# Kernel optimization log

Measured on AMD Instinct MI355X. Metric: run time of the kernel, lower is better.

Reference implementation:

```python
import jax, jax.numpy as jnp
import numpy as np

N_NODES = 20000
N_EDGES = 320000
IN_DIM = 256
OUT_DIM = 256
H1, H2 = 640, 320


def _linear_params(key, fan_in, fan_out):
    k1, k2 = jax.random.split(key)
    bound = 1.0 / np.sqrt(fan_in)
    w = jax.random.uniform(k1, (fan_in, fan_out), minval=-bound, maxval=bound, dtype=jnp.float32)
    b = jax.random.uniform(k2, (fan_out,), minval=-bound, maxval=bound, dtype=jnp.float32)
    return w, b


def setup_inputs() -> dict:
    key = jax.random.key(0)
    ks = jax.random.split(key, 10)
    features = jax.random.normal(ks[0], (N_NODES, IN_DIM), dtype=jnp.float32)
    edge_index = jax.random.randint(ks[1], (2, N_EDGES), 0, N_NODES, dtype=jnp.int64)
    w1a, b1a = _linear_params(ks[2], IN_DIM, H1)
    w1b, b1b = _linear_params(ks[3], H1, H1)
    w2a, b2a = _linear_params(ks[4], H1, H2)
    w2b, b2b = _linear_params(ks[5], H2, H2)
    w3a, b3a = _linear_params(ks[6], H2, OUT_DIM)
    w3b, b3b = _linear_params(ks[7], OUT_DIM, OUT_DIM)
    wr, br = _linear_params(ks[8], IN_DIM, OUT_DIM)
    return dict(features=features, edge_index=edge_index,
                w1a=w1a, b1a=b1a, w1b=w1b, b1b=b1b,
                w2a=w2a, b2a=b2a, w2b=w2b, b2b=b2b,
                w3a=w3a, b3a=b3a, w3b=w3b, b3b=b3b,
                wr=wr, br=br)


def _gin_layer(x, src, dst, wa, ba, wb, bb):
    # DGL GINConv 'sum': h = (1+eps)*x + sum_{src->dst} x[src], eps=0
    agg = jax.ops.segment_sum(x[src], dst, num_segments=N_NODES)
    h = x + agg
    h = jax.nn.elu(h @ wa + ba)
    h = jax.nn.elu(h @ wb + bb)
    return h


def reference(features, edge_index, w1a, b1a, w1b, b1b, w2a, b2a, w2b, b2b,
              w3a, b3a, w3b, b3b, wr, br):
    src, dst = edge_index[0], edge_index[1]
    res = jax.nn.elu(features @ wr + br)
    x = jax.nn.elu(_gin_layer(features, src, dst, w1a, b1a, w1b, b1b))
    # dropout (p=0.2) omitted: eval mode
    x = jax.nn.elu(_gin_layer(x, src, dst, w2a, b2a, w2b, b2b))
    x = _gin_layer(x, src, dst, w3a, b3a, w3b, b3b)
    return (x, res)
```

## Files before the change

### kernel.cpp

```cpp
#include <hip/hip_runtime.h>
#include <cstdint>
#include <cstddef>

#define NN 20000
#define NE 320000

typedef short short8 __attribute__((ext_vector_type(8)));
typedef float f32x4 __attribute__((ext_vector_type(4)));
typedef unsigned short u16;

__device__ __forceinline__ float b2f(u16 u) {
  union { unsigned int i; float f; } z; z.i = ((unsigned int)u) << 16; return z.f;
}
__device__ __forceinline__ u16 f2b(float f) {
  union { float f; unsigned int i; } z; z.f = f;
  unsigned int r = z.i + 0x7fffu + ((z.i >> 16) & 1u);
  return (u16)(r >> 16);
}
__device__ __forceinline__ float eluf(float v) {
  return v > 0.0f ? v : __expf(v) - 1.0f;
}

__global__ __launch_bounds__(256) void k_prep(
    const float* __restrict__ features, u16* __restrict__ xbf_sliced,
    const int* __restrict__ edst, int* __restrict__ counts,
    const float* __restrict__ wr, const float* __restrict__ w1a,
    const float* __restrict__ w1b, const float* __restrict__ w2a,
    const float* __restrict__ w2b, const float* __restrict__ w3a,
    const float* __restrict__ w3b,
    u16* __restrict__ wrt, u16* __restrict__ w1at, u16* __restrict__ w1bt,
    u16* __restrict__ w2at, u16* __restrict__ w2bt, u16* __restrict__ w3at,
    u16* __restrict__ w3bt) {
  int tid = blockIdx.x * 256 + threadIdx.x;
  if (tid < 1280000) {
    int node = tid >> 6;
    int c4 = (tid & 63) * 4;
    float4 v = *reinterpret_cast<const float4*>(features + (size_t)node * 256 + c4);
    ushort4 o;
    o.x = f2b(v.x); o.y = f2b(v.y); o.z = f2b(v.z); o.w = f2b(v.w);
    int slice = c4 >> 6, within = c4 & 63;
    *reinterpret_cast<ushort4*>(xbf_sliced + (size_t)slice * NN * 64 +
                                (size_t)node * 64 + within) = o;
    return;
  }
  if (tid < 1600000) {
    atomicAdd(&counts[edst[tid - 1280000]], 1);
    return;
  }
  int r = tid - 1600000;
  const float* Ws[7] = {wr, w1a, w1b, w2a, w2b, w3a, w3b};
  u16* Wts[7] = {wrt, w1at, w1bt, w2at, w2bt, w3at, w3bt};
  const int Kd[7] = {256, 256, 640, 640, 320, 320, 256};
  const int Nd[7] = {256, 640, 640, 320, 320, 256, 256};
  const int cnt[7] = {65536, 163840, 409600, 204800, 102400, 81920, 65536};
#pragma unroll
  for (int j = 0; j < 7; ++j) {
    if (r < cnt[j]) {
      int n = r / Kd[j], k = r - n * Kd[j];
      Wts[j][r] = f2b(Ws[j][(size_t)k * Nd[j] + n]);
      return;
    }
    r -= cnt[j];
  }
}

__global__ __launch_bounds__(1024) void k_scan(const int* __restrict__ counts,
                                               int* __restrict__ rs,
                                               int* __restrict__ cur) {
  __shared__ int wsum[16];
  __shared__ int carry_s;
  int t = threadIdx.x;
  int l = t & 63, w = t >> 6;
  if (t == 0) carry_s = 0;
  __syncthreads();
  for (int base = 0; base < NN; base += 4096) {
    int idx = base + t * 4;
    int4 v = {0, 0, 0, 0};
    if (idx < NN) v = *reinterpret_cast<const int4*>(counts + idx);
    int p0 = v.x, p1 = p0 + v.y, p2 = p1 + v.z, p3 = p2 + v.w;
    int incl = p3;
#pragma unroll
    for (int off = 1; off < 64; off <<= 1) {
      int u = __shfl_up(incl, off, 64);
      if (l >= off) incl += u;
    }
    if (l == 63) wsum[w] = incl;
    __syncthreads();
    int carry = carry_s;
    int wpre = 0;
    for (int k2 = 0; k2 < w; ++k2) wpre += wsum[k2];
    int tot = 0;
    if (t == 0)
      for (int k2 = 0; k2 < 16; ++k2) tot += wsum[k2];
    int ex = carry + wpre + incl - p3;
    if (idx < NN) {
      int4 o;
      o.x = ex; o.y = ex + p0; o.z = ex + p1; o.w = ex + p2;
      *reinterpret_cast<int4*>(rs + idx) = o;
      *reinterpret_cast<int4*>(cur + idx) = o;
    }
    __syncthreads();
    if (t == 0) carry_s = carry + tot;
    __syncthreads();
  }
  if (t == 0) rs[NN] = carry_s;
}

__global__ __launch_bounds__(256) void k_scatter(const int* __restrict__ src,
                                                 const int* __restrict__ dst,
                                                 int* __restrict__ cursor,
                                                 int* __restrict__ csr_src, int ne) {
  int i = blockIdx.x * 256 + threadIdx.x;
  if (i >= ne) return;
  int d = dst[i];
  int p = atomicAdd(&cursor[d], 1);
  csr_src[p] = src[i];
}

template <int D, int ACT>
__global__ __launch_bounds__(256) void k_agg(const u16* __restrict__ xs,
                                             const int* __restrict__ rs,
                                             const int* __restrict__ cs,
                                             const float* __restrict__ bias,
                                             u16* __restrict__ h) {
  constexpr int SW = D / 4;
  constexpr int NCs = SW / 8;
  constexpr int NPB = 256 / NCs;
  int b = blockIdx.x;
  int cls = b & 7;
  int slice = cls & 3;
  int half = cls >> 2;
  int t = threadIdx.x;
  int nl = t / NCs, ch = t - nl * NCs;
  if (nl >= NPB) return;
  int node = half * 10000 + (b >> 3) * NPB + nl;
  if (node >= (half ? NN : 10000)) return;
  const u16* xp = xs + (size_t)slice * NN * SW + (size_t)ch * 8;
  float acc[8];
  {
    short8 v = *reinterpret_cast<const short8*>(xp + (size_t)node * SW);
#pragma unroll
    for (int q = 0; q < 8; ++q) acc[q] = b2f((u16)v[q]);
  }
  int e0 = rs[node], e1 = rs[node + 1];
  int e = e0;
  for (; e + 16 <= e1; e += 16) {
    int s[16];
#pragma unroll
    for (int u = 0; u < 16; ++u) s[u] = cs[e + u];
    short8 v[16];
#pragma unroll
    for (int u = 0; u < 16; ++u)
      v[u] = *reinterpret_cast<const short8*>(xp + (size_t)s[u] * SW);
#pragma unroll
    for (int q = 0; q < 8; ++q) {
      float a0 = (b2f((u16)v[0][q]) + b2f((u16)v[1][q])) +
                 (b2f((u16)v[2][q]) + b2f((u16)v[3][q]));
      float a1 = (b2f((u16)v[4][q]) + b2f((u16)v[5][q])) +
                 (b2f((u16)v[6][q]) + b2f((u16)v[7][q]));
      float a2 = (b2f((u16)v[8][q]) + b2f((u16)v[9][q])) +
                 (b2f((u16)v[10][q]) + b2f((u16)v[11][q]));
      float a3 = (b2f((u16)v[12][q]) + b2f((u16)v[13][q])) +
                 (b2f((u16)v[14][q]) + b2f((u16)v[15][q]));
      acc[q] += (a0 + a1) + (a2 + a3);
    }
  }
  for (; e + 8 <= e1; e += 8) {
    int s[8];
#pragma unroll
    for (int u = 0; u < 8; ++u) s[u] = cs[e + u];
    short8 v[8];
#pragma unroll
    for (int u = 0; u < 8; ++u)
      v[u] = *reinterpret_cast<const short8*>(xp + (size_t)s[u] * SW);
#pragma unroll
    for (int q = 0; q < 8; ++q) {
      float a0 = b2f((u16)v[0][q]) + b2f((u16)v[1][q]);
      float a1 = b2f((u16)v[2][q]) + b2f((u16)v[3][q]);
      float a2 = b2f((u16)v[4][q]) + b2f((u16)v[5][q]);
      float a3 = b2f((u16)v[6][q]) + b2f((u16)v[7][q]);
      acc[q] += (a0 + a1) + (a2 + a3);
    }
  }
  for (; e + 4 <= e1; e += 4) {
    int s0 = cs[e], s1 = cs[e + 1], s2 = cs[e + 2], s3 = cs[e + 3];
    short8 v0 = *reinterpret_cast<const short8*>(xp + (size_t)s0 * SW);
    short8 v1 = *reinterpret_cast<const short8*>(xp + (size_t)s1 * SW);
    short8 v2 = *reinterpret_cast<const short8*>(xp + (size_t)s2 * SW);
    short8 v3 = *reinterpret_cast<const short8*>(xp + (size_t)s3 * SW);
#pragma unroll
    for (int q = 0; q < 8; ++q)
      acc[q] += (b2f((u16)v0[q]) + b2f((u16)v1[q])) + (b2f((u16)v2[q]) + b2f((u16)v3[q]));
  }
  for (; e < e1; ++e) {
    int s = cs[e];
    short8 v = *reinterpret_cast<const short8*>(xp + (size_t)s * SW);
#pragma unroll
    for (int q = 0; q < 8; ++q) acc[q] += b2f((u16)v[q]);
  }
  int col0 = slice * SW + ch * 8;
  if (ACT == 1) {
    float4 b0 = *reinterpret_cast<const float4*>(bias + col0);
    float4 b1 = *reinterpret_cast<const float4*>(bias + col0 + 4);
    acc[0] = eluf(acc[0] + b0.x); acc[1] = eluf(acc[1] + b0.y);
    acc[2] = eluf(acc[2] + b0.z); acc[3] = eluf(acc[3] + b0.w);
    acc[4] = eluf(acc[4] + b1.x); acc[5] = eluf(acc[5] + b1.y);
    acc[6] = eluf(acc[6] + b1.z); acc[7] = eluf(acc[7] + b1.w);
  }
  short8 o;
#pragma unroll
  for (int q = 0; q < 8; ++q) o[q] = (short)f2b(acc[q]);
  *reinterpret_cast<short8*>(h + (size_t)node * D + col0) = o;
}

template <int BM, int K, int N, int ACT, bool OUTF32, bool INS, int OSW, int SLOTS>
__global__ __launch_bounds__(256) void k_gemm(const u16* __restrict__ A,
                                              const u16* __restrict__ Bt,
                                              const float* __restrict__ bias,
                                              void* __restrict__ outp, int M) {
  constexpr int NBY = (N + 127) / 128;
  constexpr int NK = K / 32;
  constexpr int ABUF = BM * 32;
  constexpr int BUFSZ = ABUF + 4096;
  constexpr int MI = BM / 32;
  constexpr int LPT = BM / 64 + 2;
  __shared__ __align__(16) u16 smem[SLOTS * BUFSZ];
  int t = threadIdx.x;
  int l = t & 63, w = t >> 6;
  int lm = l & 15, lk = l >> 4;

  int nb = gridDim.x;
  int q8 = nb >> 3, r8 = nb & 7;
  int orig = blockIdx.x;
  int xcd = orig & 7, idx = orig >> 3;
  int wg = (xcd < r8 ? xcd * (q8 + 1) : r8 * (q8 + 1) + (xcd - r8) * q8) + idx;
  int m0 = (wg / NBY) * BM;
  int n0 = (wg % NBY) * 128;
  int wm = (w >> 1) * (BM / 2), wn = (w & 1) * 64;

  f32x4 acc[MI][4];
#pragma unroll
  for (int i = 0; i < MI; ++i)
#pragma unroll
    for (int j = 0; j < 4; ++j)
#pragma unroll
      for (int qq = 0; qq < 4; ++qq) acc[i][j][qq] = 0.0f;

  auto stage = [&](int buf, int kt) {
    int k0 = kt * 32;
    u16* As = smem + buf * BUFSZ;
    u16* Bs = As + ABUF;
#pragma unroll
    for (int it = 0; it < BM / 64; ++it) {
      int c = it * 256 + t;
      int row = c >> 2;
      int kc = (c & 3) ^ ((c >> 3) & 3);
      int ra = m0 + row; ra = ra < M ? ra : M - 1;
      const u16* ga;
      if (INS)
        ga = A + (size_t)(k0 >> 6) * NN * 64 + (size_t)ra * 64 + (k0 & 63) + kc * 8;
      else
        ga = A + (size_t)ra * K + k0 + kc * 8;
      __builtin_amdgcn_global_load_lds(
          (const __attribute__((address_space(1))) void*)ga,
          (__attribute__((address_space(3))) void*)(As + c * 8), 16, 0, 0);
    }
#pragma unroll
    for (int it = 0; it < 2; ++it) {
      int c = it * 256 + t;
      int row = c >> 2;
      int kc = (c & 3) ^ ((c >> 3) & 3);
      int rb = n0 + row; rb = rb < N ? rb : N - 1;
      const u16* gb = Bt + (size_t)rb * K + k0 + kc * 8;
      __builtin_amdgcn_global_load_lds(
          (const __attribute__((address_space(1))) void*)gb,
          (__attribute__((address_space(3))) void*)(Bs + c * 8), 16, 0, 0);
    }
  };

  int kidx = (lk ^ ((lm >> 1) & 3)) * 8;

#pragma unroll
  for (int s = 0; s < SLOTS; ++s) {
    stage(s, s);
    asm volatile("" ::: "memory");
  }
  int buf = 0;
  for (int kt = 0; kt < NK; ++kt) {
    int rem = NK - 1 - kt;
    if (SLOTS == 3) {
      if (rem >= 2)
        asm volatile("s_waitcnt vmcnt(%0)" ::"n"(2 * LPT) : "memory");
      else if (rem == 1)
        asm volatile("s_waitcnt vmcnt(%0)" ::"n"(LPT) : "memory");
      else
        asm volatile("s_waitcnt vmcnt(0)" ::: "memory");
    } else {
      if (rem >= 1)
        asm volatile("s_waitcnt vmcnt(%0)" ::"n"(LPT) : "memory");
      else
        asm volatile("s_waitcnt vmcnt(0)" ::: "memory");
    }
    __builtin_amdgcn_s_barrier();
    asm volatile("" ::: "memory");
    const u16* As = smem + buf * BUFSZ;
    const u16* Bs = As + ABUF;
    short8 af[MI], bf[4];
#pragma unroll
    for (int i = 0; i < MI; ++i)
      af[i] = *reinterpret_cast<const short8*>(As + (wm + i * 16 + lm) * 32 + kidx);
#pragma unroll
    for (int j = 0; j < 4; ++j)
      bf[j] = *reinterpret_cast<const short8*>(Bs + (wn + j * 16 + lm) * 32 + kidx);
    __builtin_amdgcn_s_setprio(1);
#pragma unroll
    for (int i = 0; i < MI; ++i)
#pragma unroll
      for (int j = 0; j < 4; ++j)
        acc[i][j] = __builtin_amdgcn_mfma_f32_16x16x32_bf16(af[i], bf[j], acc[i][j], 0, 0, 0);
    __builtin_amdgcn_s_setprio(0);
    asm volatile("s_waitcnt lgkmcnt(0)" ::: "memory");
    __builtin_amdgcn_s_barrier();
    asm volatile("" ::: "memory");
    if (kt + SLOTS < NK) stage(buf, kt + SLOTS);
    buf = (buf == SLOTS - 1) ? 0 : buf + 1;
  }

  if (!OUTF32) {
    u16* ep = smem + w * (BM / 2) * 64;
#pragma unroll
    for (int j = 0; j < 4; ++j) {
      int col = n0 + wn + j * 16 + lm;
      float bv = (ACT > 0) ? bias[col < N ? col : N - 1] : 0.0f;
#pragma unroll
      for (int i = 0; i < MI; ++i)
#pragma unroll
        for (int qq = 0; qq < 4; ++qq) {
          float v = acc[i][j][qq];
          if (ACT > 0) { v += bv; v = eluf(v); }
          if (ACT == 2) v = eluf(v);
          ep[(i * 16 + lk * 4 + qq) * 64 + j * 16 + lm] = f2b(v);
        }
    }
    __syncthreads();
    u16* op = (u16*)outp;
#pragma unroll
    for (int u = 0; u < BM / 16; ++u) {
      int rrow = m0 + wm + u * 8 + (l >> 3);
      int col = n0 + wn + (l & 7) * 8;
      if (rrow < M && col < N) {
        short8 val = *reinterpret_cast<const short8*>(ep + u * 512 + l * 8);
        if (OSW) {
          int slice = col / OSW, within = col - slice * OSW;
          *reinterpret_cast<short8*>(op + (size_t)slice * NN * OSW +
                                     (size_t)rrow * OSW + within) = val;
        } else {
          *reinterpret_cast<short8*>(op + (size_t)rrow * N + col) = val;
        }
      }
    }
  } else {
    float* op = (float*)outp;
#pragma unroll
    for (int j = 0; j < 4; ++j) {
      int col = n0 + wn + j * 16 + lm;
      if (col >= N) continue;
      float bv = (ACT > 0) ? bias[col] : 0.0f;
#pragma unroll
      for (int i = 0; i < MI; ++i) {
        int rb = m0 + wm + i * 16 + lk * 4;
#pragma unroll
        for (int qq = 0; qq < 4; ++qq) {
          int rr = rb + qq;
          if (rr >= M) continue;
          float v = acc[i][j][qq];
          if (ACT > 0) { v += bv; v = eluf(v); }
          if (ACT == 2) v = eluf(v);
          op[(size_t)rr * N + col] = v;
        }
      }
    }
  }
}

__global__ __launch_bounds__(256) void k_gemmd(
    const u16* __restrict__ A0, const u16* __restrict__ Bt0,
    const float* __restrict__ bias0, float* __restrict__ out0,
    const u16* __restrict__ A1, const u16* __restrict__ Bt1,
    const float* __restrict__ bias1, float* __restrict__ out1) {
  constexpr int K = 256, N = 256, BM = 64;
  constexpr int NBY = 2, NK = 8, NT0 = 626;
  constexpr int ABUF = BM * 32, BUFSZ = ABUF + 4096, MI = 2, LPT = 3;
  constexpr int SLOTS = 3;
  __shared__ __align__(16) u16 smem[SLOTS * BUFSZ];
  int t = threadIdx.x;
  int l = t & 63, w = t >> 6;
  int lm = l & 15, lk = l >> 4;

  int nb = gridDim.x;
  int q8 = nb >> 3, r8 = nb & 7;
  int orig = blockIdx.x;
  int xcd = orig & 7, idx = orig >> 3;
  int wg = (xcd < r8 ? xcd * (q8 + 1) : r8 * (q8 + 1) + (xcd - r8) * q8) + idx;
  bool second = wg >= NT0;
  int tt = second ? wg - NT0 : wg;
  const u16* A = second ? A1 : A0;
  const u16* Bt = second ? Bt1 : Bt0;
  const float* bias = second ? bias1 : bias0;
  float* op = second ? out1 : out0;

  int m0 = (tt / NBY) * BM;
  int n0 = (tt % NBY) * 128;
  int wm = (w >> 1) * (BM / 2), wn = (w & 1) * 64;

  f32x4 acc[MI][4];
#pragma unroll
  for (int i = 0; i < MI; ++i)
#pragma unroll
    for (int j = 0; j < 4; ++j)
#pragma unroll
      for (int qq = 0; qq < 4; ++qq) acc[i][j][qq] = 0.0f;

  auto stage = [&](int buf, int kt) {
    int k0 = kt * 32;
    u16* As = smem + buf * BUFSZ;
    u16* Bs = As + ABUF;
    {
      int c = t;
      int row = c >> 2;
      int kc = (c & 3) ^ ((c >> 3) & 3);
      int ra = m0 + row; ra = ra < NN ? ra : NN - 1;
      const u16* ga;
      if (second)
        ga = A + (size_t)(k0 >> 6) * NN * 64 + (size_t)ra * 64 + (k0 & 63) + kc * 8;
      else
        ga = A + (size_t)ra * K + k0 + kc * 8;
      __builtin_amdgcn_global_load_lds(
          (const __attribute__((address_space(1))) void*)ga,
          (__attribute__((address_space(3))) void*)(As + c * 8), 16, 0, 0);
    }
#pragma unroll
    for (int it = 0; it < 2; ++it) {
      int c = it * 256 + t;
      int row = c >> 2;
      int kc = (c & 3) ^ ((c >> 3) & 3);
      int rb = n0 + row; rb = rb < N ? rb : N - 1;
      const u16* gb = Bt + (size_t)rb * K + k0 + kc * 8;
      __builtin_amdgcn_global_load_lds(
          (const __attribute__((address_space(1))) void*)gb,
          (__attribute__((address_space(3))) void*)(Bs + c * 8), 16, 0, 0);
    }
  };

  int kidx = (lk ^ ((lm >> 1) & 3)) * 8;

#pragma unroll
  for (int s = 0; s < SLOTS; ++s) {
    stage(s, s);
    asm volatile("" ::: "memory");
  }
  int buf = 0;
  for (int kt = 0; kt < NK; ++kt) {
    int rem = NK - 1 - kt;
    if (rem >= 2)
      asm volatile("s_waitcnt vmcnt(%0)" ::"n"(2 * LPT) : "memory");
    else if (rem == 1)
      asm volatile("s_waitcnt vmcnt(%0)" ::"n"(LPT) : "memory");
    else
      asm volatile("s_waitcnt vmcnt(0)" ::: "memory");
    __builtin_amdgcn_s_barrier();
    asm volatile("" ::: "memory");
    const u16* As = smem + buf * BUFSZ;
    const u16* Bs = As + ABUF;
    short8 af[MI], bf[4];
#pragma unroll
    for (int i = 0; i < MI; ++i)
      af[i] = *reinterpret_cast<const short8*>(As + (wm + i * 16 + lm) * 32 + kidx);
#pragma unroll
    for (int j = 0; j < 4; ++j)
      bf[j] = *reinterpret_cast<const short8*>(Bs + (wn + j * 16 + lm) * 32 + kidx);
    __builtin_amdgcn_s_setprio(1);
#pragma unroll
    for (int i = 0; i < MI; ++i)
#pragma unroll
      for (int j = 0; j < 4; ++j)
        acc[i][j] = __builtin_amdgcn_mfma_f32_16x16x32_bf16(af[i], bf[j], acc[i][j], 0, 0, 0);
    __builtin_amdgcn_s_setprio(0);
    asm volatile("s_waitcnt lgkmcnt(0)" ::: "memory");
    __builtin_amdgcn_s_barrier();
    asm volatile("" ::: "memory");
    if (kt + SLOTS < NK) stage(buf, kt + SLOTS);
    buf = (buf == SLOTS - 1) ? 0 : buf + 1;
  }

#pragma unroll
  for (int j = 0; j < 4; ++j) {
    int col = n0 + wn + j * 16 + lm;
    float bv = bias[col];
#pragma unroll
    for (int i = 0; i < MI; ++i) {
      int rb = m0 + wm + i * 16 + lk * 4;
#pragma unroll
      for (int qq = 0; qq < 4; ++qq) {
        int rr = rb + qq;
        if (rr >= NN) continue;
        float v = eluf(acc[i][j][qq] + bv);
        op[(size_t)rr * N + col] = v;
      }
    }
  }
}

extern "C" void kernel_launch(void* const* d_in, const int* in_sizes, int n_in,
                              void* d_out, int out_size, void* d_ws, size_t ws_size,
                              hipStream_t stream) {
  const float* features = (const float*)d_in[0];
  const int* eidx = (const int*)d_in[1];
  const float* w1a = (const float*)d_in[2];
  const float* b1a = (const float*)d_in[3];
  const float* w1b = (const float*)d_in[4];
  const float* b1b = (const float*)d_in[5];
  const float* w2a = (const float*)d_in[6];
  const float* b2a = (const float*)d_in[7];
  const float* w2b = (const float*)d_in[8];
  const float* b2b = (const float*)d_in[9];
  const float* w3a = (const float*)d_in[10];
  const float* b3a = (const float*)d_in[11];
  const float* w3b = (const float*)d_in[12];
  const float* b3b = (const float*)d_in[13];
  const float* wr = (const float*)d_in[14];
  const float* br = (const float*)d_in[15];

  char* ws = (char*)d_ws;
  u16* bufX = (u16*)(ws);
  u16* bufA = (u16*)(ws + 10240000);
  u16* bufB = (u16*)(ws + 35840000);
  u16* wrt = (u16*)(ws + 61440000);
  u16* w1at = wrt + 256 * 256;
  u16* w1bt = w1at + 640 * 256;
  u16* w2at = w1bt + 640 * 640;
  u16* w2bt = w2at + 320 * 640;
  u16* w3at = w2bt + 320 * 320;
  u16* w3bt = w3at + 256 * 320;
  int* row_start = (int*)(ws + 63700992);
  int* cursor = row_start + 20004;
  int* csr_src = cursor + NN;
  int* counts = csr_src + NE;

  const int* esrc = eidx;
  const int* edst = eidx + NE;

  hipMemsetAsync(counts, 0, NN * sizeof(int), stream);
  k_prep<<<10523, 256, 0, stream>>>(features, bufX, edst, counts, wr, w1a, w1b,
                                    w2a, w2b, w3a, w3b, wrt, w1at, w1bt, w2at,
                                    w2bt, w3at, w3bt);
  k_scan<<<1, 1024, 0, stream>>>(counts, row_start, cursor);
  k_scatter<<<(NE + 255) / 256, 256, 0, stream>>>(esrc, edst, cursor, csr_src, NE);

  float* out_x = (float*)d_out;
  float* out_res = (float*)d_out + (size_t)NN * 256;

  k_agg<256, 0><<<8 * 313, 256, 0, stream>>>(bufX, row_start, csr_src, nullptr, bufA);
  k_gemm<128, 256, 640, 1, false, false, 0, 2><<<dim3(157 * 5), 256, 0, stream>>>(bufA, w1at, b1a, bufB, NN);
  k_gemm<128, 640, 640, 2, false, false, 0, 2><<<dim3(157 * 5), 256, 0, stream>>>(bufB, w1bt, b1b, bufA, NN);
  k_gemm<128, 640, 320, 0, false, false, 80, 3><<<dim3(157 * 3), 256, 0, stream>>>(bufA, w2at, nullptr, bufB, NN);
  k_agg<320, 1><<<8 * 400, 256, 0, stream>>>(bufB, row_start, csr_src, b2a, bufA);
  k_gemm<64, 320, 320, 2, false, false, 0, 3><<<dim3(313 * 3), 256, 0, stream>>>(bufA, w2bt, b2b, bufB, NN);
  k_gemm<64, 320, 256, 0, false, false, 64, 3><<<dim3(313 * 2), 256, 0, stream>>>(bufB, w3at, nullptr, bufA, NN);
  k_agg<256, 1><<<8 * 313, 256, 0, stream>>>(bufA, row_start, csr_src, b3a, bufB);
  k_gemmd<<<dim3(626 * 2), 256, 0, stream>>>(bufB, w3bt, b3b, out_x,
                                             bufX, wrt, br, out_res);
}
```

Before: 245.4 us.

## Sort nodes by degree for aggregation load balance and reduce GEMM pipeline slots

Builds a degree histogram in the scan kernel and a counting-sort permutation of nodes by in-degree in the scatter kernel. Aggregation kernels then process nodes in permuted order, so threads in a block see similar degrees and waste less time on divergence. Separately, the last two layer GEMMs and the dual GEMM drop from three to two LDS pipeline slots, with adjusted waitcnts, trading prefetch depth for occupancy. The permutation work is extra, and the scattered output order may hurt write locality.

```diff
diff --git a/kernel.cpp b/kernel.cpp
--- a/kernel.cpp
+++ b/kernel.cpp
@@ -66,17 +66,26 @@
 
 __global__ __launch_bounds__(1024) void k_scan(const int* __restrict__ counts,
                                                int* __restrict__ rs,
-                                               int* __restrict__ cur) {
+                                               int* __restrict__ cur,
+                                               int* __restrict__ dcur) {
   __shared__ int wsum[16];
   __shared__ int carry_s;
+  __shared__ int wh[16][256];
   int t = threadIdx.x;
   int l = t & 63, w = t >> 6;
   if (t == 0) carry_s = 0;
+  for (int i = t; i < 16 * 256; i += 1024) ((int*)wh)[i] = 0;
   __syncthreads();
   for (int base = 0; base < NN; base += 4096) {
     int idx = base + t * 4;
     int4 v = {0, 0, 0, 0};
-    if (idx < NN) v = *reinterpret_cast<const int4*>(counts + idx);
+    if (idx < NN) {
+      v = *reinterpret_cast<const int4*>(counts + idx);
+      atomicAdd(&wh[w][v.x < 255 ? v.x : 255], 1);
+      atomicAdd(&wh[w][v.y < 255 ? v.y : 255], 1);
+      atomicAdd(&wh[w][v.z < 255 ? v.z : 255], 1);
+      atomicAdd(&wh[w][v.w < 255 ? v.w : 255], 1);
+    }
     int p0 = v.x, p1 = p0 + v.y, p2 = p1 + v.z, p3 = p2 + v.w;
     int incl = p3;
 #pragma unroll
@@ -104,23 +113,54 @@
     __syncthreads();
   }
   if (t == 0) rs[NN] = carry_s;
+  __syncthreads();
+  int dv = 0, incl = 0;
+  if (t < 256) {
+    int s = 0;
+#pragma unroll
+    for (int k2 = 0; k2 < 16; ++k2) s += wh[k2][t];
+    dv = s;
+    incl = s;
+#pragma unroll
+    for (int off = 1; off < 64; off <<= 1) {
+      int u = __shfl_up(incl, off, 64);
+      if (l >= off) incl += u;
+    }
+    if (l == 63) wsum[w] = incl;
+  }
+  __syncthreads();
+  if (t < 256) {
+    int basew = 0;
+    for (int k2 = 0; k2 < w; ++k2) basew += wsum[k2];
+    dcur[t] = basew + incl - dv;
+  }
 }
 
 __global__ __launch_bounds__(256) void k_scatter(const int* __restrict__ src,
                                                  const int* __restrict__ dst,
                                                  int* __restrict__ cursor,
-                                                 int* __restrict__ csr_src, int ne) {
+                                                 int* __restrict__ csr_src,
+                                                 const int* __restrict__ counts,
+                                                 int* __restrict__ dcur,
+                                                 int* __restrict__ perm) {
   int i = blockIdx.x * 256 + threadIdx.x;
-  if (i >= ne) return;
-  int d = dst[i];
-  int p = atomicAdd(&cursor[d], 1);
-  csr_src[p] = src[i];
+  if (i < NE) {
+    int d = dst[i];
+    int p = atomicAdd(&cursor[d], 1);
+    csr_src[p] = src[i];
+  } else if (i < NE + NN) {
+    int nd = i - NE;
+    int deg = counts[nd]; if (deg > 255) deg = 255;
+    int p = atomicAdd(&dcur[deg], 1);
+    perm[p] = nd;
+  }
 }
 
 template <int D, int ACT>
 __global__ __launch_bounds__(256) void k_agg(const u16* __restrict__ xs,
                                              const int* __restrict__ rs,
                                              const int* __restrict__ cs,
+                                             const int* __restrict__ perm,
                                              const float* __restrict__ bias,
                                              u16* __restrict__ h) {
   constexpr int SW = D / 4;
@@ -133,8 +173,9 @@
   int t = threadIdx.x;
   int nl = t / NCs, ch = t - nl * NCs;
   if (nl >= NPB) return;
-  int node = half * 10000 + (b >> 3) * NPB + nl;
-  if (node >= (half ? NN : 10000)) return;
+  int idx2 = (b >> 3) * NPB + nl;
+  if (idx2 >= 10000) return;
+  int node = perm[idx2 * 2 + half];
   const u16* xp = xs + (size_t)slice * NN * SW + (size_t)ch * 8;
   float acc[8];
   {
@@ -391,7 +432,7 @@
   constexpr int K = 256, N = 256, BM = 64;
   constexpr int NBY = 2, NK = 8, NT0 = 626;
   constexpr int ABUF = BM * 32, BUFSZ = ABUF + 4096, MI = 2, LPT = 3;
-  constexpr int SLOTS = 3;
+  constexpr int SLOTS = 2;
   __shared__ __align__(16) u16 smem[SLOTS * BUFSZ];
   int t = threadIdx.x;
   int l = t & 63, w = t >> 6;
@@ -462,9 +503,7 @@
   int buf = 0;
   for (int kt = 0; kt < NK; ++kt) {
     int rem = NK - 1 - kt;
-    if (rem >= 2)
-      asm volatile("s_waitcnt vmcnt(%0)" ::"n"(2 * LPT) : "memory");
-    else if (rem == 1)
+    if (rem >= 1)
       asm volatile("s_waitcnt vmcnt(%0)" ::"n"(LPT) : "memory");
     else
       asm volatile("s_waitcnt vmcnt(0)" ::: "memory");
@@ -546,6 +585,8 @@
   int* cursor = row_start + 20004;
   int* csr_src = cursor + NN;
   int* counts = csr_src + NE;
+  int* dcur = counts + NN;
+  int* perm = dcur + 256;
 
   const int* esrc = eidx;
   const int* edst = eidx + NE;
@@ -554,20 +595,21 @@
   k_prep<<<10523, 256, 0, stream>>>(features, bufX, edst, counts, wr, w1a, w1b,
                                     w2a, w2b, w3a, w3b, wrt, w1at, w1bt, w2at,
                                     w2bt, w3at, w3bt);
-  k_scan<<<1, 1024, 0, stream>>>(counts, row_start, cursor);
-  k_scatter<<<(NE + 255) / 256, 256, 0, stream>>>(esrc, edst, cursor, csr_src, NE);
+  k_scan<<<1, 1024, 0, stream>>>(counts, row_start, cursor, dcur);
+  k_scatter<<<(NE + NN + 255) / 256, 256, 0, stream>>>(esrc, edst, cursor,
+                                                       csr_src, counts, dcur, perm);
 
   float* out_x = (float*)d_out;
   float* out_res = (float*)d_out + (size_t)NN * 256;
 
-  k_agg<256, 0><<<8 * 313, 256, 0, stream>>>(bufX, row_start, csr_src, nullptr, bufA);
+  k_agg<256, 0><<<8 * 313, 256, 0, stream>>>(bufX, row_start, csr_src, perm, nullptr, bufA);
   k_gemm<128, 256, 640, 1, false, false, 0, 2><<<dim3(157 * 5), 256, 0, stream>>>(bufA, w1at, b1a, bufB, NN);
   k_gemm<128, 640, 640, 2, false, false, 0, 2><<<dim3(157 * 5), 256, 0, stream>>>(bufB, w1bt, b1b, bufA, NN);
   k_gemm<128, 640, 320, 0, false, false, 80, 3><<<dim3(157 * 3), 256, 0, stream>>>(bufA, w2at, nullptr, bufB, NN);
-  k_agg<320, 1><<<8 * 400, 256, 0, stream>>>(bufB, row_start, csr_src, b2a, bufA);
-  k_gemm<64, 320, 320, 2, false, false, 0, 3><<<dim3(313 * 3), 256, 0, stream>>>(bufA, w2bt, b2b, bufB, NN);
-  k_gemm<64, 320, 256, 0, false, false, 64, 3><<<dim3(313 * 2), 256, 0, stream>>>(bufB, w3at, nullptr, bufA, NN);
-  k_agg<256, 1><<<8 * 313, 256, 0, stream>>>(bufA, row_start, csr_src, b3a, bufB);
+  k_agg<320, 1><<<8 * 400, 256, 0, stream>>>(bufB, row_start, csr_src, perm, b2a, bufA);
+  k_gemm<64, 320, 320, 2, false, false, 0, 2><<<dim3(313 * 3), 256, 0, stream>>>(bufA, w2bt, b2b, bufB, NN);
+  k_gemm<64, 320, 256, 0, false, false, 64, 2><<<dim3(313 * 2), 256, 0, stream>>>(bufB, w3at, nullptr, bufA, NN);
+  k_agg<256, 1><<<8 * 313, 256, 0, stream>>>(bufA, row_start, csr_src, perm, b3a, bufB);
   k_gemmd<<<dim3(626 * 2), 256, 0, stream>>>(bufB, w3bt, b3b, out_x,
                                              bufX, wrt, br, out_res);
 }
```

Result: slower. 292.8 us (+19.3%).
